# Performance work log

Hardware: AMD Instinct MI355X
Metric: run time of the kernel (lower is better)

The kernel has to match this reference:

```python
import jax, jax.numpy as jnp
import numpy as np

EPS = 1e-5

def _mlp(x, w1, b1, w2, b2):
    # torch: Linear -> ReLU -> Linear (weights stored as (in, out))
    return jax.nn.relu(x @ w1 + b1) @ w2 + b2

def _ln(x, g, b):
    mu = x.mean(-1, keepdims=True)
    var = ((x - mu) ** 2).mean(-1, keepdims=True)
    return (x - mu) * jax.lax.rsqrt(var + EPS) * g + b

def setup_inputs():
    key = jax.random.key(0)
    B, N, d, d_out, M, K = 8, 8192, 256, 512, 2048, 16
    ks = jax.random.split(key, 16)
    def nrm(k, shape, s=0.05):
        return jax.random.normal(k, shape, jnp.float32) * s
    return dict(
        pos=jax.random.normal(ks[0], (B, N, 3), jnp.float32),
        feat=jax.random.normal(ks[1], (B, N, d), jnp.float32),
        fps_idx=jax.random.randint(ks[2], (B, M), 0, N, jnp.int32),
        knn_idx=jax.random.randint(ks[3], (B, M, K), 0, N, jnp.int32),
        cs1=16, cs2=64,
        mlp1_w1=nrm(ks[4], (2, 4, d), 0.3), mlp1_b1=jnp.zeros((2, d)),
        mlp1_w2=nrm(ks[5], (2, d, d)), mlp1_b2=jnp.zeros((2, d)),
        mlp2_w1=nrm(ks[6], (2, 6, d), 0.3), mlp2_b1=jnp.zeros((2, d)),
        mlp2_w2=nrm(ks[7], (2, d, d)), mlp2_b2=jnp.zeros((2, d)),
        wq=nrm(ks[8], (2, d, d)), wk=nrm(ks[9], (2, d, d)),
        wv=nrm(ks[10], (2, d, d)), wo=nrm(ks[11], (2, d, d)), bo=jnp.zeros((2, d)),
        ln_g=jnp.ones((2, d)), ln_b=jnp.zeros((2, d)),
        td_w=nrm(ks[12], (d, d_out)), td_b=jnp.zeros((d_out,)),
        bn_g=jnp.ones((d_out,)), bn_b=jnp.zeros((d_out,)),
        bn_mean=jnp.zeros((d_out,)), bn_var=jnp.ones((d_out,)),
    )

def reference(pos, feat, fps_idx, knn_idx, cs1, cs2,
              mlp1_w1, mlp1_b1, mlp1_w2, mlp1_b2,
              mlp2_w1, mlp2_b1, mlp2_w2, mlp2_b2,
              wq, wk, wv, wo, bo, ln_g, ln_b,
              td_w, td_b, bn_g, bn_b, bn_mean, bn_var):
    def block(f_in, cs, i):
        # DLPTBlock with equal-size contiguous clusters of size cs.
        # Note: original forward returns ln1(h_pos + dlsa_out); the ff branch is dead code.
        B, N, d = f_in.shape
        nc = N // cs
        pc = pos.reshape(B, nc, cs, 3)
        fc = f_in.reshape(B, nc, cs, d)
        cog = pc.mean(axis=2, keepdims=True)         # per-cluster center of gravity
        lp = pc - cog                                # local coords
        nrm = jnp.linalg.norm(lp, axis=-1, keepdims=True)
        h_pos = fc + _mlp(jnp.concatenate([lp, nrm], -1),
                          mlp1_w1[i], mlp1_b1[i], mlp1_w2[i], mlp1_b2[i])
        avg = jnp.broadcast_to(lp.mean(axis=2, keepdims=True), lp.shape)
        h_geo = fc + _mlp(jnp.concatenate([avg, lp], -1),
                          mlp2_w1[i], mlp2_b1[i], mlp2_w2[i], mlp2_b2[i])
        q = (h_geo @ wq[i]) / jnp.sqrt(jnp.float32(d))
        k = h_geo @ wk[i]
        v = h_pos @ wv[i]
        a = jax.nn.softmax(jnp.einsum('bcqd,bckd->bcqk', q, k), axis=-1)
        out = jnp.einsum('bcqk,bckd->bcqd', a, v) @ wo[i] + bo[i]
        return _ln(h_pos + out, ln_g[i], ln_b[i]).reshape(B, N, d)

    f = block(feat, cs1, 0)
    f = block(f, cs2, 1)
    # TransitionDown: linear -> BN (eval, running stats) -> relu -> knn max-pool
    f = f @ td_w + td_b
    f = jax.nn.relu((f - bn_mean) * jax.lax.rsqrt(bn_var + EPS) * bn_g + bn_b)
    pos_ds = jnp.take_along_axis(pos, fps_idx[..., None], axis=1)   # (B, M, 3)
    B = f.shape[0]
    f_knn = f[jnp.arange(B)[:, None, None], knn_idx]                # (B, M, K, d_out)
    feat_ds = f_knn.max(axis=2)
    return (pos_ds, feat_ds)
```

## Files before the change

### kernel.cpp

```cpp
#include <hip/hip_runtime.h>
#include <stdint.h>
#include <stddef.h>

typedef __attribute__((ext_vector_type(8))) short bf16x8;
typedef __attribute__((ext_vector_type(4))) float f32x4;
typedef __attribute__((ext_vector_type(8))) unsigned short u16x8;
typedef __attribute__((ext_vector_type(4))) unsigned short u16x4;
typedef __attribute__((ext_vector_type(2))) unsigned short u16x2;

#define DEVINL __device__ __forceinline__

DEVINL unsigned short f2b(float x){
  union { float f; unsigned int u; } v; v.f = x;
  return (unsigned short)((v.u + 0x7FFFu + ((v.u >> 16) & 1u)) >> 16);
}
DEVINL float b2f(unsigned short h){
  union { float f; unsigned int u; } v; v.u = ((unsigned int)h) << 16;
  return v.f;
}

DEVINL void gl_lds16(void* g, void* lds){
  __builtin_amdgcn_global_load_lds(
      (__attribute__((address_space(1))) void*)g,
      (__attribute__((address_space(3))) void*)lds, 16, 0, 0);
}

__global__ __launch_bounds__(256) void prep_k(
    const float* __restrict__ m1w2, const float* __restrict__ m2w2,
    const float* __restrict__ wqp,  const float* __restrict__ wkp,
    const float* __restrict__ wvp,  const float* __restrict__ wop,
    const float* __restrict__ tdw,  const float* __restrict__ tdb,
    const float* __restrict__ bng,  const float* __restrict__ bnb,
    const float* __restrict__ bnm,  const float* __restrict__ bnv,
    unsigned short* __restrict__ wT, float* __restrict__ bns, float* __restrict__ bnt)
{
  int idx = blockIdx.x * 256 + threadIdx.x;
  if (idx < 786432){
    int mat = idx >> 17;
    int e   = idx & 131071;
    int i   = e >> 16;
    int eb  = e & 65535;
    int n = eb >> 8, kx = eb & 255;
    const float* src; float sc = 1.0f;
    if      (mat == 0) src = m1w2;
    else if (mat == 1) src = m2w2;
    else if (mat == 2){ src = wqp; sc = 0.0625f; }
    else if (mat == 3) src = wkp;
    else if (mat == 4) src = wvp;
    else               src = wop;
    wT[idx] = f2b(src[i*65536 + kx*256 + n] * sc);
  } else if (idx < 917504){
    int e = idx - 786432;
    int n = e >> 8, kx = e & 255;
    wT[786432 + e] = f2b(tdw[kx*512 + n]);
  } else if (idx < 918016){
    int c = idx - 917504;
    float s = bng[c] * rsqrtf(bnv[c] + 1e-5f);
    bns[c] = s;
    bnt[c] = (tdb[c] - bnm[c]) * s + bnb[c];
  }
}

__global__ __launch_bounds__(256) void gemm_k(
    const unsigned short* __restrict__ A,
    const unsigned short* __restrict__ Wt,
    unsigned short* __restrict__ out,
    const float* __restrict__ bias,
    const unsigned short* __restrict__ addend,
    const float* __restrict__ bn_s,
    const float* __restrict__ bn_t,
    int ldc)
{
  __shared__ __attribute__((aligned(16))) unsigned short aT[512*8];
  __shared__ __attribute__((aligned(16))) unsigned short bT[512*8];
  __shared__ __attribute__((aligned(16))) unsigned short epi[128*140];

  const int tid  = threadIdx.x;
  const int lane = tid & 63;
  const int wave = tid >> 6;
  const int lrow = lane & 15, lq = lane >> 4;
  const int wr = wave >> 1, wc = wave & 1;
  const int m0 = blockIdx.x * 128;
  const int n0 = blockIdx.y * 128;

  f32x4 acc[4][4] = {};

  int aOff[4], bOff[4];
#pragma unroll
  for (int mt = 0; mt < 4; mt++){
    int row = wr*64 + mt*16 + lrow;
    aOff[mt] = row*64 + ((lq ^ ((row >> 1) & 3)) << 4);
  }
#pragma unroll
  for (int nt = 0; nt < 4; nt++){
    int row = wc*64 + nt*16 + lrow;
    bOff[nt] = row*64 + ((lq ^ ((row >> 1) & 3)) << 4);
  }

  const int s0 = tid, s1 = tid + 256;
  const int r0 = s0 >> 2, kc0 = (s0 & 3) ^ ((r0 >> 1) & 3);
  const int r1 = s1 >> 2, kc1 = (s1 & 3) ^ ((r1 >> 1) & 3);
  const unsigned short* Ab = A  + (size_t)m0 * 256;
  const unsigned short* Bb = Wt + (size_t)n0 * 256;
  char* aL = (char*)aT;
  char* bL = (char*)bT;
  const int wslot = wave * 64 * 16;

  for (int k0 = 0; k0 < 256; k0 += 32){
    __syncthreads();
    gl_lds16((void*)(Ab + r0*256 + k0 + kc0*8), aL + wslot);
    gl_lds16((void*)(Ab + r1*256 + k0 + kc1*8), aL + 4096 + wslot);
    gl_lds16((void*)(Bb + r0*256 + k0 + kc0*8), bL + wslot);
    gl_lds16((void*)(Bb + r1*256 + k0 + kc1*8), bL + 4096 + wslot);
    __syncthreads();
    bf16x8 af[4], bfr[4];
#pragma unroll
    for (int mt = 0; mt < 4; mt++) af[mt]  = *(const bf16x8*)(aL + aOff[mt]);
#pragma unroll
    for (int nt = 0; nt < 4; nt++) bfr[nt] = *(const bf16x8*)(bL + bOff[nt]);
#pragma unroll
    for (int mt = 0; mt < 4; mt++)
#pragma unroll
      for (int nt = 0; nt < 4; nt++)
        acc[mt][nt] = __builtin_amdgcn_mfma_f32_16x16x32_bf16(af[mt], bfr[nt], acc[mt][nt], 0, 0, 0);
  }

  __syncthreads();
#pragma unroll
  for (int mt = 0; mt < 4; mt++){
    int row = wr*64 + mt*16 + lq*4;
#pragma unroll
    for (int nt = 0; nt < 4; nt++){
      int col = wc*64 + nt*16 + lrow;
#pragma unroll
      for (int r = 0; r < 4; r++)
        epi[(row + r)*140 + col] = f2b(acc[mt][nt][r]);
    }
  }
  __syncthreads();

  const int erow = tid >> 1, h = tid & 1;
  const size_t gbase = (size_t)(m0 + erow) * (size_t)ldc + n0;
#pragma unroll
  for (int i = 0; i < 8; i++){
    int col = h*64 + i*8;
    u16x4 lo = *(const u16x4*)(&epi[erow*140 + col]);
    u16x4 hi = *(const u16x4*)(&epi[erow*140 + col + 4]);
    float y[8];
#pragma unroll
    for (int j = 0; j < 4; j++){ y[j] = b2f(lo[j]); y[4+j] = b2f(hi[j]); }
    if (addend){
      u16x8 ad = *(const u16x8*)(addend + gbase + col);
#pragma unroll
      for (int j = 0; j < 8; j++) y[j] += b2f(ad[j]);
    }
    if (bias){
#pragma unroll
      for (int j = 0; j < 8; j++) y[j] += bias[n0 + col + j];
    }
    if (bn_s){
#pragma unroll
      for (int j = 0; j < 8; j++){
        float t2 = y[j]*bn_s[n0 + col + j] + bn_t[n0 + col + j];
        y[j] = fmaxf(t2, 0.f);
      }
    }
    u16x8 o;
#pragma unroll
    for (int j = 0; j < 8; j++) o[j] = f2b(y[j]);
    *(u16x8*)(out + gbase + col) = o;
  }
}

DEVINL void wg_gemm_reg(const unsigned short* __restrict__ Wt,
                        const unsigned short* Als, int tid, f32x4 (&acc)[4][2])
{
  const int lane = tid & 63;
  const int wave = tid >> 6;
  const int lrow = lane & 15, lq = lane >> 4;
  const unsigned short* base[2];
#pragma unroll
  for (int nt = 0; nt < 2; nt++)
    base[nt] = Wt + (size_t)(wave*32 + nt*16 + lrow)*256 + lq*8;

  bf16x8 breg[8][2];
#pragma unroll
  for (int k = 0; k < 8; k++)
#pragma unroll
    for (int nt = 0; nt < 2; nt++)
      breg[k][nt] = *(const bf16x8*)(base[nt] + k*32);

#pragma unroll
  for (int k = 0; k < 8; k++){
    bf16x8 af[4];
#pragma unroll
    for (int mt = 0; mt < 4; mt++)
      af[mt] = *(const bf16x8*)(Als + (mt*16 + lrow)*264 + k*32 + lq*8);
#pragma unroll
    for (int mt = 0; mt < 4; mt++)
#pragma unroll
      for (int nt = 0; nt < 2; nt++)
        acc[mt][nt] = __builtin_amdgcn_mfma_f32_16x16x32_bf16(af[mt], breg[k][nt], acc[mt][nt], 0, 0, 0);
  }
}

DEVINL void wg_epi(f32x4 (&acc)[4][2], unsigned short* Yls,
                   const unsigned short* resls, const float* __restrict__ bias, int tid)
{
  const int lane = tid & 63, wave = tid >> 6;
  const int lrow = lane & 15, lq = lane >> 4;
#pragma unroll
  for (int mt = 0; mt < 4; mt++){
#pragma unroll
    for (int nt = 0; nt < 2; nt++){
      int col = wave*32 + nt*16 + lrow;
#pragma unroll
      for (int r = 0; r < 4; r++){
        int row = mt*16 + lq*4 + r;
        float y = acc[mt][nt][r];
        if (bias) y += bias[col];
        if (resls) y += b2f(resls[row*264 + col]);
        Yls[row*264 + col] = f2b(y);
      }
    }
  }
  __syncthreads();
}

DEVINL void wg_epi_vt(f32x4 (&acc)[4][2], unsigned short* VT, int tid)
{
  const int lane = tid & 63, wave = tid >> 6;
  const int lrow = lane & 15, lq = lane >> 4;
#pragma unroll
  for (int mt = 0; mt < 4; mt++){
#pragma unroll
    for (int nt = 0; nt < 2; nt++){
      int col = wave*32 + nt*16 + lrow;
      int row0 = mt*16 + lq*4;
      u16x4 w;
#pragma unroll
      for (int r = 0; r < 4; r++) w[r] = f2b(acc[mt][nt][r]);
      *(u16x4*)(VT + col*72 + row0) = w;
    }
  }
  __syncthreads();
}

template<int CS, bool F32IN>
__global__ __launch_bounds__(512, 2) void block_k(
    const float* __restrict__ pos,
    const float* __restrict__ featF,
    const unsigned short* __restrict__ featB,
    const float* __restrict__ w1a, const float* __restrict__ b1a,
    const float* __restrict__ w1b, const float* __restrict__ b1b,
    const unsigned short* __restrict__ m1w2T, const float* __restrict__ m1b2,
    const unsigned short* __restrict__ m2w2T, const float* __restrict__ m2b2,
    const unsigned short* __restrict__ wqT, const unsigned short* __restrict__ wkT,
    const unsigned short* __restrict__ wvT, const unsigned short* __restrict__ woT,
    const float* __restrict__ bo, const float* __restrict__ lgam,
    const float* __restrict__ lbet,
    unsigned short* __restrict__ out)
{
  __shared__ __attribute__((aligned(16))) char smem[135168];
  __shared__ float P3[64][3];
  __shared__ float Cg[4][3];
  __shared__ float Gg[64][4];
  __shared__ float sred[64][8];
  __shared__ float s2red[64][8];
  __shared__ float mub[64];
  __shared__ float rsb[64];

  unsigned short* B0 = (unsigned short*)(smem);
  unsigned short* B1 = (unsigned short*)(smem + 33792);
  unsigned short* B2 = (unsigned short*)(smem + 67584);
  unsigned short* B3 = (unsigned short*)(smem + 101376);
  constexpr int SS = (CS == 64) ? 66 : 18;
  constexpr int PS = (CS == 64) ? 72 : 40;
  float* Sb = (float*)B3;
  unsigned short* Pb = (unsigned short*)((char*)B3 + 64*SS*4);
  unsigned short* VT = B0;

  const int tid  = threadIdx.x;
  const int lane = tid & 63;
  const int wave = tid >> 6;
  const int lrow = lane & 15, lq = lane >> 4;
  const int m0 = blockIdx.x * 64;

  if (tid < 64){
    P3[tid][0] = pos[(size_t)(m0+tid)*3 + 0];
    P3[tid][1] = pos[(size_t)(m0+tid)*3 + 1];
    P3[tid][2] = pos[(size_t)(m0+tid)*3 + 2];
  }
  {
    const int row = tid >> 3, cb = (tid & 7) * 32;
    if (F32IN){
      const float* src = featF + (size_t)(m0 + row)*256 + cb;
#pragma unroll
      for (int i = 0; i < 4; i++){
        float4 a = *(const float4*)(src + i*8);
        float4 b = *(const float4*)(src + i*8 + 4);
        u16x8 o;
        o[0]=f2b(a.x); o[1]=f2b(a.y); o[2]=f2b(a.z); o[3]=f2b(a.w);
        o[4]=f2b(b.x); o[5]=f2b(b.y); o[6]=f2b(b.z); o[7]=f2b(b.w);
        *(u16x8*)(B0 + row*264 + cb + i*8) = o;
      }
    } else {
      const unsigned short* src = featB + (size_t)(m0 + row)*256 + cb;
#pragma unroll
      for (int i = 0; i < 4; i++)
        *(u16x8*)(B0 + row*264 + cb + i*8) = *(const u16x8*)(src + i*8);
    }
  }
  __syncthreads();

  constexpr int NCH = 64 / CS;
  if (tid < NCH*3){
    int ch = tid / 3, c = tid - ch*3;
    float s = 0.f;
    for (int r = 0; r < CS; r++) s += P3[ch*CS + r][c];
    Cg[ch][c] = s / (float)CS;
  }
  __syncthreads();
  if (tid < 64){
    int ch = (CS == 16) ? (tid >> 4) : 0;
    float x = P3[tid][0] - Cg[ch][0];
    float y = P3[tid][1] - Cg[ch][1];
    float z = P3[tid][2] - Cg[ch][2];
    Gg[tid][0] = x; Gg[tid][1] = y; Gg[tid][2] = z;
    Gg[tid][3] = sqrtf(x*x + y*y + z*z);
  }
  __syncthreads();

  {
    const int c = tid & 255;
    const int r0 = (tid >> 8) * 32;
    const float wa0 = w1a[c], wa1 = w1a[256+c], wa2 = w1a[512+c], wa3 = w1a[768+c];
    const float ba  = b1a[c];
    for (int r = r0; r < r0 + 32; r++){
      float v1 = ba + Gg[r][0]*wa0 + Gg[r][1]*wa1 + Gg[r][2]*wa2 + Gg[r][3]*wa3;
      B1[r*264 + c] = f2b(fmaxf(v1, 0.f));
    }
  }
  __syncthreads();
  {
    f32x4 acc[4][2] = {};
    wg_gemm_reg(m1w2T, B1, tid, acc);
    wg_epi(acc, B2, B0, m1b2, tid);
  }
  {
    const int c = tid & 255;
    const int r0 = (tid >> 8) * 32;
    const float wb0 = w1b[768+c], wb1 = w1b[1024+c], wb2 = w1b[1280+c];
    const float bb  = b1b[c];
    for (int r = r0; r < r0 + 32; r++){
      float v2 = bb + Gg[r][0]*wb0 + Gg[r][1]*wb1 + Gg[r][2]*wb2;
      B1[r*264 + c] = f2b(fmaxf(v2, 0.f));
    }
  }
  __syncthreads();
  {
    f32x4 acc[4][2] = {};
    wg_gemm_reg(m2w2T, B1, tid, acc);
    wg_epi(acc, B3, B0, m2b2, tid);
  }
  {
    f32x4 acc[4][2] = {};
    wg_gemm_reg(wqT, B3, tid, acc);
    wg_epi(acc, B0, nullptr, nullptr, tid);
  }
  {
    f32x4 acc[4][2] = {};
    wg_gemm_reg(wkT, B3, tid, acc);
    wg_epi(acc, B1, nullptr, nullptr, tid);
  }

  if (CS == 64){
    const int tr = wave & 3, tc0 = wave >> 2;
    f32x4 sacc[2] = {};
    const int qrow = tr*16 + lrow;
#pragma unroll
    for (int kk = 0; kk < 8; kk++){
      bf16x8 aq = *(const bf16x8*)(B0 + qrow*264 + kk*32 + lq*8);
#pragma unroll
      for (int c = 0; c < 2; c++){
        int brow = (tc0 + c*2)*16 + lrow;
        bf16x8 bk = *(const bf16x8*)(B1 + brow*264 + kk*32 + lq*8);
        sacc[c] = __builtin_amdgcn_mfma_f32_16x16x32_bf16(aq, bk, sacc[c], 0, 0, 0);
      }
    }
#pragma unroll
    for (int c = 0; c < 2; c++)
#pragma unroll
      for (int r = 0; r < 4; r++)
        Sb[(tr*16 + lq*4 + r)*SS + (tc0 + c*2)*16 + lrow] = sacc[c][r];
  } else {
    if (wave < 4){
      f32x4 sacc = {};
      const int qrow = wave*16 + lrow;
#pragma unroll
      for (int kk = 0; kk < 8; kk++){
        bf16x8 aq = *(const bf16x8*)(B0 + qrow*264 + kk*32 + lq*8);
        bf16x8 bk = *(const bf16x8*)(B1 + qrow*264 + kk*32 + lq*8);
        sacc = __builtin_amdgcn_mfma_f32_16x16x32_bf16(aq, bk, sacc, 0, 0, 0);
      }
#pragma unroll
      for (int r = 0; r < 4; r++)
        Sb[(wave*16 + lq*4 + r)*SS + lrow] = sacc[r];
    }
  }
  __syncthreads();

  if (tid < 64){
    float mx = -3.0e38f;
    for (int j = 0; j < CS; j++) mx = fmaxf(mx, Sb[tid*SS + j]);
    float sum = 0.f;
    for (int j = 0; j < CS; j++){
      float e = __expf(Sb[tid*SS + j] - mx);
      Sb[tid*SS + j] = e; sum += e;
    }
    float inv = 1.0f / sum;
    for (int j = 0; j < CS; j++) Pb[tid*PS + j] = f2b(Sb[tid*SS + j] * inv);
    if (CS == 16){
      for (int j = 16; j < 32; j++) Pb[tid*PS + j] = 0;
    }
  }
  __syncthreads();

  {
    f32x4 acc[4][2] = {};
    wg_gemm_reg(wvT, B2, tid, acc);
    wg_epi_vt(acc, VT, tid);
  }

  {
    f32x4 oacc[4][2] = {};
    const int dbase = wave * 32;
    if (CS == 64){
#pragma unroll
      for (int kk = 0; kk < 2; kk++){
        bf16x8 ap[4];
#pragma unroll
        for (int mt = 0; mt < 4; mt++)
          ap[mt] = *(const bf16x8*)(Pb + (mt*16 + lrow)*PS + kk*32 + lq*8);
#pragma unroll
        for (int nt = 0; nt < 2; nt++){
          const int d = dbase + nt*16 + lrow;
          bf16x8 bv = *(const bf16x8*)(VT + d*72 + kk*32 + lq*8);
#pragma unroll
          for (int mt = 0; mt < 4; mt++)
            oacc[mt][nt] = __builtin_amdgcn_mfma_f32_16x16x32_bf16(ap[mt], bv, oacc[mt][nt], 0, 0, 0);
        }
      }
    } else {
#pragma unroll
      for (int mt = 0; mt < 4; mt++){
        bf16x8 ap = *(const bf16x8*)(Pb + (mt*16 + lrow)*PS + lq*8);
#pragma unroll
        for (int nt = 0; nt < 2; nt++){
          const int d = dbase + nt*16 + lrow;
          bf16x8 bv = *(const bf16x8*)(VT + d*72 + mt*16 + (lq & 1)*8);
          oacc[mt][nt] = __builtin_amdgcn_mfma_f32_16x16x32_bf16(ap, bv, oacc[mt][nt], 0, 0, 0);
        }
      }
    }
    __syncthreads();
#pragma unroll
    for (int mt = 0; mt < 4; mt++){
#pragma unroll
      for (int nt = 0; nt < 2; nt++){
#pragma unroll
        for (int r = 0; r < 4; r++){
          int row = mt*16 + lq*4 + r;
          int col = dbase + nt*16 + lrow;
          B1[row*264 + col] = f2b(oacc[mt][nt][r]);
        }
      }
    }
  }
  __syncthreads();

  {
    f32x4 acc[4][2] = {};
    wg_gemm_reg(woT, B1, tid, acc);
    wg_epi(acc, B0, nullptr, nullptr, tid);
  }
  {
    const int row = tid >> 3, part = tid & 7;
    const size_t gr = (size_t)(m0 + row) * 256;
    float sm = 0.f, sq = 0.f;
#pragma unroll
    for (int i = 0; i < 4; i++){
      int col = part*32 + i*8;
      u16x8 v  = *(const u16x8*)(B0 + row*264 + col);
      u16x8 rr = *(const u16x8*)(B2 + row*264 + col);
      u16x8 w;
#pragma unroll
      for (int j = 0; j < 8; j++){
        float y = b2f(v[j]) + bo[col + j] + b2f(rr[j]);
        sm += y; sq += y*y;
        w[j] = f2b(y);
      }
      *(u16x8*)(B0 + row*264 + col) = w;
    }
    sred[row][part] = sm; s2red[row][part] = sq;
    __syncthreads();
    if (tid < 64){
      float s = 0.f, q2 = 0.f;
#pragma unroll
      for (int p = 0; p < 8; p++){ s += sred[tid][p]; q2 += s2red[tid][p]; }
      float mu = s * (1.0f/256.0f);
      float var = q2 * (1.0f/256.0f) - mu*mu;
      mub[tid] = mu;
      rsb[tid] = rsqrtf(var + 1e-5f);
    }
    __syncthreads();
    const float mu = mub[row], rs = rsb[row];
#pragma unroll
    for (int i = 0; i < 4; i++){
      int col = part*32 + i*8;
      u16x8 v = *(const u16x8*)(B0 + row*264 + col);
      u16x8 o;
#pragma unroll
      for (int j = 0; j < 8; j++)
        o[j] = f2b((b2f(v[j]) - mu)*rs*lgam[col + j] + lbet[col + j]);
      *(u16x8*)(out + gr + col) = o;
    }
  }
}

__global__ __launch_bounds__(256) void out_k(
    const unsigned short* __restrict__ F2,
    const float* __restrict__ pos,
    const int* __restrict__ fps,
    const int* __restrict__ knn,
    float* __restrict__ outp)
{
  const int p = blockIdx.x;
  const int b = p >> 11;
  const int t = threadIdx.x;
  const int* kn = knn + (size_t)p * 16;
  const int c = t * 2;
  float m1 = -3.0e38f, m2 = -3.0e38f;
  for (int j = 0; j < 16; j++){
    int idx = kn[j];
    size_t row = ((size_t)b * 8192 + idx) * 512;
    u16x2 v = *(const u16x2*)(F2 + row + c);
    m1 = fmaxf(m1, b2f(v.x));
    m2 = fmaxf(m2, b2f(v.y));
  }
  float* of = outp + 49152 + (size_t)p * 512 + c;
  float2 o; o.x = m1; o.y = m2;
  *(float2*)of = o;
  if (t < 3){
    int fi = fps[p];
    outp[(size_t)p*3 + t] = pos[((size_t)b*8192 + fi)*3 + t];
  }
}

extern "C" void kernel_launch(void* const* d_in, const int* in_sizes, int n_in,
                              void* d_out, int out_size, void* d_ws, size_t ws_size,
                              hipStream_t stream)
{
  (void)in_sizes; (void)n_in; (void)out_size; (void)ws_size;

  const float* pos  = (const float*)d_in[0];
  const float* feat = (const float*)d_in[1];
  const int*   fps  = (const int*)d_in[2];
  const int*   knn  = (const int*)d_in[3];
  const float* m1w1 = (const float*)d_in[6];
  const float* m1b1 = (const float*)d_in[7];
  const float* m1w2 = (const float*)d_in[8];
  const float* m1b2 = (const float*)d_in[9];
  const float* m2w1 = (const float*)d_in[10];
  const float* m2b1 = (const float*)d_in[11];
  const float* m2w2 = (const float*)d_in[12];
  const float* m2b2 = (const float*)d_in[13];
  const float* wq   = (const float*)d_in[14];
  const float* wk   = (const float*)d_in[15];
  const float* wv   = (const float*)d_in[16];
  const float* wo   = (const float*)d_in[17];
  const float* bo   = (const float*)d_in[18];
  const float* lng  = (const float*)d_in[19];
  const float* lnb  = (const float*)d_in[20];
  const float* tdw  = (const float*)d_in[21];
  const float* tdb  = (const float*)d_in[22];
  const float* bng  = (const float*)d_in[23];
  const float* bnb  = (const float*)d_in[24];
  const float* bnm  = (const float*)d_in[25];
  const float* bnv  = (const float*)d_in[26];

  char* ws = (char*)d_ws;
  unsigned short* wT = (unsigned short*)ws;
  float* bns = (float*)(ws + 1835008);
  float* bnt = (float*)(ws + 1837056);
  const size_t SLOT = 33554432;
  unsigned short* A  = (unsigned short*)(ws + 2097152);
  unsigned short* Bs = (unsigned short*)(ws + 2097152 + SLOT);
  unsigned short* E  = (unsigned short*)(ws + 2097152 + 2*SLOT);

  auto wtm = [&](int mat, int i){ return wT + (size_t)mat*131072 + (size_t)i*65536; };
  unsigned short* tdT = wT + 786432;

  prep_k<<<3586, 256, 0, stream>>>(m1w2, m2w2, wq, wk, wv, wo, tdw, tdb, bng, bnb, bnm, bnv,
                                   wT, bns, bnt);

  block_k<16, true><<<1024, 512, 0, stream>>>(
      pos, feat, nullptr,
      m1w1, m1b1, m2w1, m2b1,
      wtm(0,0), m1b2, wtm(1,0), m2b2,
      wtm(2,0), wtm(3,0), wtm(4,0), wtm(5,0),
      bo, lng, lnb, A);

  block_k<64, false><<<1024, 512, 0, stream>>>(
      pos, nullptr, A,
      m1w1 + 1024, m1b1 + 256, m2w1 + 1536, m2b1 + 256,
      wtm(0,1), m1b2 + 256, wtm(1,1), m2b2 + 256,
      wtm(2,1), wtm(3,1), wtm(4,1), wtm(5,1),
      bo + 256, lng + 256, lnb + 256, Bs);

  gemm_k<<<dim3(512,4), 256, 0, stream>>>(Bs, tdT, E, nullptr, nullptr, bns, bnt, 512);

  out_k<<<16384, 256, 0, stream>>>(E, pos, fps, knn, (float*)d_out);
}
```

Measured before the change: 623.5 us.

## Shrink LDS footprint with XOR-swizzled buffers to fit four blocks per CU

Replaces the four padded 33 KB LDS buffers with two unpadded 32 KB buffers that use an XOR row swizzle to avoid bank conflicts. This cuts shared memory from about 135 KB to about 81 KB and raises launch bounds to 4 blocks per CU. Residual inputs are read straight from global memory instead of being staged in LDS. h_pos is spilled to the output buffer in global memory and reloaded later, and the GEMM order is rearranged so buffers can be reused. Softmax now runs in registers using shuffle reductions, with a small cross-wave merge for CS=64. The cost is extra global round-trips for h_pos and the residual, more syncs, and a risk of register spills under the tighter launch bound.

```diff
diff --git a/kernel.cpp b/kernel.cpp
--- a/kernel.cpp
+++ b/kernel.cpp
@@ -173,7 +173,7 @@
 }
 
 DEVINL void wg_gemm_reg(const unsigned short* __restrict__ Wt,
-                        const unsigned short* Als, int tid, f32x4 (&acc)[4][2])
+                        const char* Als, int tid, f32x4 (&acc)[4][2])
 {
   const int lane = tid & 63;
   const int wave = tid >> 6;
@@ -190,12 +190,19 @@
     for (int nt = 0; nt < 2; nt++)
       breg[k][nt] = *(const bf16x8*)(base[nt] + k*32);
 
+  int rbase[4], rsw[4];
+#pragma unroll
+  for (int mt = 0; mt < 4; mt++){
+    int row = mt*16 + lrow;
+    rbase[mt] = row*512;
+    rsw[mt]   = (row & 7) << 4;
+  }
 #pragma unroll
   for (int k = 0; k < 8; k++){
     bf16x8 af[4];
 #pragma unroll
     for (int mt = 0; mt < 4; mt++)
-      af[mt] = *(const bf16x8*)(Als + (mt*16 + lrow)*264 + k*32 + lq*8);
+      af[mt] = *(const bf16x8*)(Als + rbase[mt] + ((k*64 + lq*16) ^ rsw[mt]));
 #pragma unroll
     for (int mt = 0; mt < 4; mt++)
 #pragma unroll
@@ -204,8 +211,12 @@
   }
 }
 
-DEVINL void wg_epi(f32x4 (&acc)[4][2], unsigned short* Yls,
-                   const unsigned short* resls, const float* __restrict__ bias, int tid)
+template<bool F32RES>
+DEVINL void wg_epi(f32x4 (&acc)[4][2], char* Yls,
+                   const float* __restrict__ resF,
+                   const unsigned short* __restrict__ resB,
+                   const float* __restrict__ bias,
+                   int tid)
 {
   const int lane = tid & 63, wave = tid >> 6;
   const int lrow = lane & 15, lq = lane >> 4;
@@ -213,21 +224,22 @@
   for (int mt = 0; mt < 4; mt++){
 #pragma unroll
     for (int nt = 0; nt < 2; nt++){
-      int col = wave*32 + nt*16 + lrow;
+      const int col = wave*32 + nt*16 + lrow;
 #pragma unroll
       for (int r = 0; r < 4; r++){
-        int row = mt*16 + lq*4 + r;
+        const int row = mt*16 + lq*4 + r;
         float y = acc[mt][nt][r];
         if (bias) y += bias[col];
-        if (resls) y += b2f(resls[row*264 + col]);
-        Yls[row*264 + col] = f2b(y);
-      }
-    }
-  }
-  __syncthreads();
-}
-
-DEVINL void wg_epi_vt(f32x4 (&acc)[4][2], unsigned short* VT, int tid)
+        if (F32RES){ if (resF) y += resF[row*256 + col]; }
+        else       { if (resB) y += b2f(resB[row*256 + col]); }
+        *(unsigned short*)(Yls + row*512 + ((col*2) ^ ((row & 7) << 4))) = f2b(y);
+      }
+    }
+  }
+  __syncthreads();
+}
+
+DEVINL void wg_epi_vt(f32x4 (&acc)[4][2], char* VT, int tid)
 {
   const int lane = tid & 63, wave = tid >> 6;
   const int lrow = lane & 15, lq = lane >> 4;
@@ -235,19 +247,19 @@
   for (int mt = 0; mt < 4; mt++){
 #pragma unroll
     for (int nt = 0; nt < 2; nt++){
-      int col = wave*32 + nt*16 + lrow;
-      int row0 = mt*16 + lq*4;
+      const int col  = wave*32 + nt*16 + lrow;
+      const int row0 = mt*16 + lq*4;
       u16x4 w;
 #pragma unroll
       for (int r = 0; r < 4; r++) w[r] = f2b(acc[mt][nt][r]);
-      *(u16x4*)(VT + col*72 + row0) = w;
+      *(u16x4*)(VT + col*128 + ((row0*2) ^ ((col & 7) << 4))) = w;
     }
   }
   __syncthreads();
 }
 
 template<int CS, bool F32IN>
-__global__ __launch_bounds__(512, 2) void block_k(
+__global__ __launch_bounds__(512, 4) void block_k(
     const float* __restrict__ pos,
     const float* __restrict__ featF,
     const unsigned short* __restrict__ featB,
@@ -261,24 +273,19 @@
     const float* __restrict__ lbet,
     unsigned short* __restrict__ out)
 {
-  __shared__ __attribute__((aligned(16))) char smem[135168];
-  __shared__ float P3[64][3];
-  __shared__ float Cg[4][3];
-  __shared__ float Gg[64][4];
-  __shared__ float sred[64][8];
-  __shared__ float s2red[64][8];
-  __shared__ float mub[64];
-  __shared__ float rsb[64];
-
-  unsigned short* B0 = (unsigned short*)(smem);
-  unsigned short* B1 = (unsigned short*)(smem + 33792);
-  unsigned short* B2 = (unsigned short*)(smem + 67584);
-  unsigned short* B3 = (unsigned short*)(smem + 101376);
-  constexpr int SS = (CS == 64) ? 66 : 18;
-  constexpr int PS = (CS == 64) ? 72 : 40;
-  float* Sb = (float*)B3;
-  unsigned short* Pb = (unsigned short*)((char*)B3 + 64*SS*4);
-  unsigned short* VT = B0;
+  __shared__ __attribute__((aligned(16))) char smem[81216];
+  char* BA = smem;
+  char* BB = smem + 32768;
+  char* Pm = smem + 65536;
+  float (*P3)[3]    = (float(*)[3])(smem + 73728);
+  float (*Cg)[3]    = (float(*)[3])(smem + 74496);
+  float (*Gg)[4]    = (float(*)[4])(smem + 74560);
+  float (*smx)[2]   = (float(*)[2])(smem + 75584);
+  float (*ssm)[2]   = (float(*)[2])(smem + 76096);
+  float (*sred)[8]  = (float(*)[8])(smem + 76608);
+  float (*s2red)[8] = (float(*)[8])(smem + 78656);
+  float* mub = (float*)(smem + 80704);
+  float* rsb = (float*)(smem + 80960);
 
   const int tid  = threadIdx.x;
   const int lane = tid & 63;
@@ -286,30 +293,16 @@
   const int lrow = lane & 15, lq = lane >> 4;
   const int m0 = blockIdx.x * 64;
 
+  const float* resFp = nullptr;
+  const unsigned short* resBp = nullptr;
+  if constexpr (F32IN) resFp = featF + (size_t)m0 * 256;
+  else                 resBp = featB + (size_t)m0 * 256;
+  unsigned short* gout = out + (size_t)m0 * 256;
+
   if (tid < 64){
     P3[tid][0] = pos[(size_t)(m0+tid)*3 + 0];
     P3[tid][1] = pos[(size_t)(m0+tid)*3 + 1];
     P3[tid][2] = pos[(size_t)(m0+tid)*3 + 2];
-  }
-  {
-    const int row = tid >> 3, cb = (tid & 7) * 32;
-    if (F32IN){
-      const float* src = featF + (size_t)(m0 + row)*256 + cb;
-#pragma unroll
-      for (int i = 0; i < 4; i++){
-        float4 a = *(const float4*)(src + i*8);
-        float4 b = *(const float4*)(src + i*8 + 4);
-        u16x8 o;
-        o[0]=f2b(a.x); o[1]=f2b(a.y); o[2]=f2b(a.z); o[3]=f2b(a.w);
-        o[4]=f2b(b.x); o[5]=f2b(b.y); o[6]=f2b(b.z); o[7]=f2b(b.w);
-        *(u16x8*)(B0 + row*264 + cb + i*8) = o;
-      }
-    } else {
-      const unsigned short* src = featB + (size_t)(m0 + row)*256 + cb;
-#pragma unroll
-      for (int i = 0; i < 4; i++)
-        *(u16x8*)(B0 + row*264 + cb + i*8) = *(const u16x8*)(src + i*8);
-    }
   }
   __syncthreads();
 
@@ -334,102 +327,155 @@
   {
     const int c = tid & 255;
     const int r0 = (tid >> 8) * 32;
+    const float wb0 = w1b[768+c], wb1 = w1b[1024+c], wb2 = w1b[1280+c];
+    const float bb  = b1b[c];
+    for (int r = r0; r < r0 + 32; r++){
+      float v2 = bb + Gg[r][0]*wb0 + Gg[r][1]*wb1 + Gg[r][2]*wb2;
+      *(unsigned short*)(BA + r*512 + ((c*2) ^ ((r & 7) << 4))) = f2b(fmaxf(v2, 0.f));
+    }
+  }
+  __syncthreads();
+  {
+    f32x4 acc[4][2] = {};
+    wg_gemm_reg(m2w2T, BA, tid, acc);
+    wg_epi<F32IN>(acc, BB, resFp, resBp, m2b2, tid);
+  }
+  {
+    const int c = tid & 255;
+    const int r0 = (tid >> 8) * 32;
     const float wa0 = w1a[c], wa1 = w1a[256+c], wa2 = w1a[512+c], wa3 = w1a[768+c];
     const float ba  = b1a[c];
     for (int r = r0; r < r0 + 32; r++){
       float v1 = ba + Gg[r][0]*wa0 + Gg[r][1]*wa1 + Gg[r][2]*wa2 + Gg[r][3]*wa3;
-      B1[r*264 + c] = f2b(fmaxf(v1, 0.f));
+      *(unsigned short*)(BA + r*512 + ((c*2) ^ ((r & 7) << 4))) = f2b(fmaxf(v1, 0.f));
     }
   }
   __syncthreads();
   {
     f32x4 acc[4][2] = {};
-    wg_gemm_reg(m1w2T, B1, tid, acc);
-    wg_epi(acc, B2, B0, m1b2, tid);
-  }
-  {
-    const int c = tid & 255;
-    const int r0 = (tid >> 8) * 32;
-    const float wb0 = w1b[768+c], wb1 = w1b[1024+c], wb2 = w1b[1280+c];
-    const float bb  = b1b[c];
-    for (int r = r0; r < r0 + 32; r++){
-      float v2 = bb + Gg[r][0]*wb0 + Gg[r][1]*wb1 + Gg[r][2]*wb2;
-      B1[r*264 + c] = f2b(fmaxf(v2, 0.f));
-    }
+    wg_gemm_reg(m1w2T, BA, tid, acc);
+    __syncthreads();
+    wg_epi<F32IN>(acc, BA, resFp, resBp, m1b2, tid);
+  }
+  {
+    const int row = tid >> 3, cb = (tid & 7) * 32;
+    const int sw = (row & 7) << 4;
+    unsigned short* dst = gout + (size_t)row*256 + cb;
+#pragma unroll
+    for (int i = 0; i < 4; i++)
+      *(u16x8*)(dst + i*8) = *(const u16x8*)(BA + row*512 + ((cb*2 + i*16) ^ sw));
   }
   __syncthreads();
   {
     f32x4 acc[4][2] = {};
-    wg_gemm_reg(m2w2T, B1, tid, acc);
-    wg_epi(acc, B3, B0, m2b2, tid);
+    wg_gemm_reg(wqT, BB, tid, acc);
+    wg_epi<false>(acc, BA, nullptr, nullptr, nullptr, tid);
   }
   {
     f32x4 acc[4][2] = {};
-    wg_gemm_reg(wqT, B3, tid, acc);
-    wg_epi(acc, B0, nullptr, nullptr, tid);
-  }
-  {
-    f32x4 acc[4][2] = {};
-    wg_gemm_reg(wkT, B3, tid, acc);
-    wg_epi(acc, B1, nullptr, nullptr, tid);
+    wg_gemm_reg(wkT, BB, tid, acc);
+    __syncthreads();
+    wg_epi<false>(acc, BB, nullptr, nullptr, nullptr, tid);
   }
 
   if (CS == 64){
     const int tr = wave & 3, tc0 = wave >> 2;
     f32x4 sacc[2] = {};
     const int qrow = tr*16 + lrow;
+    const int qsw  = (qrow & 7) << 4;
 #pragma unroll
     for (int kk = 0; kk < 8; kk++){
-      bf16x8 aq = *(const bf16x8*)(B0 + qrow*264 + kk*32 + lq*8);
+      bf16x8 aq = *(const bf16x8*)(BA + qrow*512 + ((kk*64 + lq*16) ^ qsw));
 #pragma unroll
       for (int c = 0; c < 2; c++){
-        int brow = (tc0 + c*2)*16 + lrow;
-        bf16x8 bk = *(const bf16x8*)(B1 + brow*264 + kk*32 + lq*8);
+        int brow = tc0*16 + c*32 + lrow;
+        bf16x8 bk = *(const bf16x8*)(BB + brow*512 + ((kk*64 + lq*16) ^ ((brow & 7) << 4)));
         sacc[c] = __builtin_amdgcn_mfma_f32_16x16x32_bf16(aq, bk, sacc[c], 0, 0, 0);
       }
     }
-#pragma unroll
-    for (int c = 0; c < 2; c++)
-#pragma unroll
-      for (int r = 0; r < 4; r++)
-        Sb[(tr*16 + lq*4 + r)*SS + (tc0 + c*2)*16 + lrow] = sacc[c][r];
+    float fmx[4], fsm[4];
+#pragma unroll
+    for (int r = 0; r < 4; r++){
+      float m = fmaxf(sacc[0][r], sacc[1][r]);
+#pragma unroll
+      for (int d = 1; d < 16; d <<= 1) m = fmaxf(m, __shfl_xor(m, d));
+      float e0 = __expf(sacc[0][r] - m);
+      float e1 = __expf(sacc[1][r] - m);
+      sacc[0][r] = e0; sacc[1][r] = e1;
+      float s = e0 + e1;
+#pragma unroll
+      for (int d = 1; d < 16; d <<= 1) s += __shfl_xor(s, d);
+      fmx[r] = m; fsm[r] = s;
+    }
+    if (lrow == 0){
+#pragma unroll
+      for (int r = 0; r < 4; r++){
+        int row = tr*16 + lq*4 + r;
+        smx[row][tc0] = fmx[r];
+        ssm[row][tc0] = fsm[r];
+      }
+    }
+    __syncthreads();
+#pragma unroll
+    for (int r = 0; r < 4; r++){
+      int row = tr*16 + lq*4 + r;
+      float m0v = smx[row][0], m1v = smx[row][1];
+      float M = fmaxf(m0v, m1v);
+      float S = ssm[row][0]*__expf(m0v - M) + ssm[row][1]*__expf(m1v - M);
+      float f = __expf((tc0 ? m1v : m0v) - M) / S;
+      int sw = (row & 7) << 4;
+#pragma unroll
+      for (int c = 0; c < 2; c++){
+        int col = tc0*16 + c*32 + lrow;
+        *(unsigned short*)(Pm + row*128 + ((col*2) ^ sw)) = f2b(sacc[c][r]*f);
+      }
+    }
+    __syncthreads();
   } else {
     if (wave < 4){
       f32x4 sacc = {};
       const int qrow = wave*16 + lrow;
+      const int qsw  = (qrow & 7) << 4;
 #pragma unroll
       for (int kk = 0; kk < 8; kk++){
-        bf16x8 aq = *(const bf16x8*)(B0 + qrow*264 + kk*32 + lq*8);
-        bf16x8 bk = *(const bf16x8*)(B1 + qrow*264 + kk*32 + lq*8);
+        bf16x8 aq = *(const bf16x8*)(BA + qrow*512 + ((kk*64 + lq*16) ^ qsw));
+        bf16x8 bk = *(const bf16x8*)(BB + qrow*512 + ((kk*64 + lq*16) ^ qsw));
         sacc = __builtin_amdgcn_mfma_f32_16x16x32_bf16(aq, bk, sacc, 0, 0, 0);
       }
 #pragma unroll
-      for (int r = 0; r < 4; r++)
-        Sb[(wave*16 + lq*4 + r)*SS + lrow] = sacc[r];
-    }
-  }
-  __syncthreads();
-
-  if (tid < 64){
-    float mx = -3.0e38f;
-    for (int j = 0; j < CS; j++) mx = fmaxf(mx, Sb[tid*SS + j]);
-    float sum = 0.f;
-    for (int j = 0; j < CS; j++){
-      float e = __expf(Sb[tid*SS + j] - mx);
-      Sb[tid*SS + j] = e; sum += e;
-    }
-    float inv = 1.0f / sum;
-    for (int j = 0; j < CS; j++) Pb[tid*PS + j] = f2b(Sb[tid*SS + j] * inv);
-    if (CS == 16){
-      for (int j = 16; j < 32; j++) Pb[tid*PS + j] = 0;
-    }
-  }
-  __syncthreads();
-
+      for (int r = 0; r < 4; r++){
+        float m = sacc[r];
+#pragma unroll
+        for (int d = 1; d < 16; d <<= 1) m = fmaxf(m, __shfl_xor(m, d));
+        float e = __expf(sacc[r] - m);
+        float s = e;
+#pragma unroll
+        for (int d = 1; d < 16; d <<= 1) s += __shfl_xor(s, d);
+        int row = wave*16 + lq*4 + r;
+        *(unsigned short*)(Pm + row*64 + ((lrow*2) ^ ((row & 3) << 4))) = f2b(e / s);
+      }
+    } else {
+      int t2 = tid - 256;
+      int row = t2 >> 2, j = t2 & 3;
+      u16x4 z = {};
+      *(u16x4*)(Pm + row*64 + ((32 + j*8) ^ ((row & 3) << 4))) = z;
+    }
+    __syncthreads();
+  }
+
+  {
+    const int row = tid >> 3, cb = (tid & 7) * 32;
+    const unsigned short* src = gout + (size_t)row*256 + cb;
+    const int sw = (row & 7) << 4;
+#pragma unroll
+    for (int i = 0; i < 4; i++)
+      *(u16x8*)(BA + row*512 + ((cb*2 + i*16) ^ sw)) = *(const u16x8*)(src + i*8);
+  }
+  __syncthreads();
   {
     f32x4 acc[4][2] = {};
-    wg_gemm_reg(wvT, B2, tid, acc);
-    wg_epi_vt(acc, VT, tid);
+    wg_gemm_reg(wvT, BA, tid, acc);
+    wg_epi_vt(acc, BB, tid);
   }
 
   {
@@ -440,12 +486,14 @@
       for (int kk = 0; kk < 2; kk++){
         bf16x8 ap[4];
 #pragma unroll
-        for (int mt = 0; mt < 4; mt++)
-          ap[mt] = *(const bf16x8*)(Pb + (mt*16 + lrow)*PS + kk*32 + lq*8);
+        for (int mt = 0; mt < 4; mt++){
+          int row = mt*16 + lrow;
+          ap[mt] = *(const bf16x8*)(Pm + row*128 + ((kk*64 + lq*16) ^ ((row & 7) << 4)));
+        }
 #pragma unroll
         for (int nt = 0; nt < 2; nt++){
           const int d = dbase + nt*16 + lrow;
-          bf16x8 bv = *(const bf16x8*)(VT + d*72 + kk*32 + lq*8);
+          bf16x8 bv = *(const bf16x8*)(BB + d*128 + ((kk*64 + lq*16) ^ ((d & 7) << 4)));
 #pragma unroll
           for (int mt = 0; mt < 4; mt++)
             oacc[mt][nt] = __builtin_amdgcn_mfma_f32_16x16x32_bf16(ap[mt], bv, oacc[mt][nt], 0, 0, 0);
@@ -454,11 +502,12 @@
     } else {
 #pragma unroll
       for (int mt = 0; mt < 4; mt++){
-        bf16x8 ap = *(const bf16x8*)(Pb + (mt*16 + lrow)*PS + lq*8);
+        int row = mt*16 + lrow;
+        bf16x8 ap = *(const bf16x8*)(Pm + row*64 + ((lq*16) ^ ((row & 3) << 4)));
 #pragma unroll
         for (int nt = 0; nt < 2; nt++){
           const int d = dbase + nt*16 + lrow;
-          bf16x8 bv = *(const bf16x8*)(VT + d*72 + mt*16 + (lq & 1)*8);
+          bf16x8 bv = *(const bf16x8*)(BB + d*128 + ((mt*32 + (lq & 1)*16) ^ ((d & 7) << 4)));
           oacc[mt][nt] = __builtin_amdgcn_mfma_f32_16x16x32_bf16(ap, bv, oacc[mt][nt], 0, 0, 0);
         }
       }
@@ -472,27 +521,28 @@
         for (int r = 0; r < 4; r++){
           int row = mt*16 + lq*4 + r;
           int col = dbase + nt*16 + lrow;
-          B1[row*264 + col] = f2b(oacc[mt][nt][r]);
+          *(unsigned short*)(BA + row*512 + ((col*2) ^ ((row & 7) << 4))) = f2b(oacc[mt][nt][r]);
         }
       }
     }
-  }
-  __syncthreads();
+    __syncthreads();
+  }
 
   {
     f32x4 acc[4][2] = {};
-    wg_gemm_reg(woT, B1, tid, acc);
-    wg_epi(acc, B0, nullptr, nullptr, tid);
+    wg_gemm_reg(woT, BA, tid, acc);
+    wg_epi<false>(acc, BB, nullptr, nullptr, nullptr, tid);
   }
   {
     const int row = tid >> 3, part = tid & 7;
-    const size_t gr = (size_t)(m0 + row) * 256;
+    const size_t gr = (size_t)row * 256;
+    const int sw = (row & 7) << 4;
     float sm = 0.f, sq = 0.f;
 #pragma unroll
     for (int i = 0; i < 4; i++){
       int col = part*32 + i*8;
-      u16x8 v  = *(const u16x8*)(B0 + row*264 + col);
-      u16x8 rr = *(const u16x8*)(B2 + row*264 + col);
+      u16x8 v  = *(const u16x8*)(BB + row*512 + ((col*2) ^ sw));
+      u16x8 rr = *(const u16x8*)(gout + gr + col);
       u16x8 w;
 #pragma unroll
       for (int j = 0; j < 8; j++){
@@ -500,7 +550,7 @@
         sm += y; sq += y*y;
         w[j] = f2b(y);
       }
-      *(u16x8*)(B0 + row*264 + col) = w;
+      *(u16x8*)(BB + row*512 + ((col*2) ^ sw)) = w;
     }
     sred[row][part] = sm; s2red[row][part] = sq;
     __syncthreads();
@@ -518,12 +568,12 @@
 #pragma unroll
     for (int i = 0; i < 4; i++){
       int col = part*32 + i*8;
-      u16x8 v = *(const u16x8*)(B0 + row*264 + col);
+      u16x8 v = *(const u16x8*)(BB + row*512 + ((col*2) ^ sw));
       u16x8 o;
 #pragma unroll
       for (int j = 0; j < 8; j++)
         o[j] = f2b((b2f(v[j]) - mu)*rs*lgam[col + j] + lbet[col + j]);
-      *(u16x8*)(out + gr + col) = o;
+      *(u16x8*)(gout + gr + col) = o;
     }
   }
 }
```

Result: slower. 734.5 us (+17.8%).
